# Performance work log

Hardware: AMD Instinct MI355X
Metric: run time of the kernel (lower is better)

## Reference

```python
import jax, jax.numpy as jnp
import numpy as np

B, H, S, D = 1, 16, 2048, 128
NUM_DOCS = 4


def setup_inputs() -> dict:
    key = jax.random.key(0)
    kq, kk, kv = jax.random.split(key, 3)
    q = jax.random.normal(kq, (B, H, S, D), dtype=jnp.float32)
    k = jax.random.normal(kk, (B, H, S, D), dtype=jnp.float32)
    v = jax.random.normal(kv, (B, H, S, D), dtype=jnp.float32)
    # Document boundaries within the packed sequence (as produced by _get_offsets):
    # starts at 0, ends at total token count. 4 equal docs of length 512.
    offsets = jnp.array([0, 512, 1024, 1536, 2048], dtype=jnp.int64)
    return {"q": q, "k": k, "v": v, "offsets": offsets}


def reference(q, k, v, offsets):
    # Block-causal SDPA: token i attends to token j iff j <= i and both are
    # in the same document (documents delimited by `offsets`). This matches
    # nested-tensor SDPA with is_causal=True over the jagged documents.
    _, _, S_, D_ = q.shape
    pos = jnp.arange(S_)
    seg = jnp.searchsorted(offsets, pos, side="right")  # [S] document id per token
    mask = (seg[:, None] == seg[None, :]) & (pos[None, :] <= pos[:, None])  # [S,S]
    scale = 1.0 / jnp.sqrt(jnp.asarray(D_, q.dtype))
    scores = jnp.einsum("bhsd,bhtd->bhst", q, k) * scale  # [B,H,S,S]
    scores = jnp.where(mask[None, None], scores, jnp.finfo(q.dtype).min)
    attn = jax.nn.softmax(scores, axis=-1)
    return jnp.einsum("bhst,bhtd->bhsd", attn, v)
```

## Files before the change

kernel.cpp:

```cpp
#include <hip/hip_runtime.h>
#include <hip/hip_bf16.h>
#include <math.h>

#define NH 16
#define SL 2048
#define DM 128

typedef float f32x4 __attribute__((ext_vector_type(4)));
typedef short s16x8 __attribute__((ext_vector_type(8)));
typedef short s16x4 __attribute__((ext_vector_type(4)));
typedef int   i32x4 __attribute__((ext_vector_type(4)));

static __device__ __forceinline__ unsigned short f2bfu(float f) {
  __hip_bfloat16 h = __float2bfloat16(f);
  return (unsigned short)__builtin_bit_cast(short, h);
}
static __device__ __forceinline__ short f2bf(float f) {
  __hip_bfloat16 h = __float2bfloat16(f);
  return __builtin_bit_cast(short, h);
}
static __device__ __forceinline__ unsigned pack2(float lo, float hi) {
  return (unsigned)f2bfu(lo) | ((unsigned)f2bfu(hi) << 16);
}

__global__ __launch_bounds__(256) void attn_dbuf(
    const float* __restrict__ qg,
    const float* __restrict__ kg,
    const float* __restrict__ vg,
    const int* __restrict__ offs, int n_off,
    float* __restrict__ out)
{
  __shared__ __align__(16) char Kb[2][16384];
  __shared__ __align__(16) char Vb[2][16384];

  const int t    = threadIdx.x;
  const int lane = t & 63;
  const int w    = t >> 6;
  const int col  = lane & 15;
  const int g    = lane >> 4;

  const int blk = blockIdx.x;
  const int z   = blk >> 8;
  const int y   = (blk >> 4) & 15;
  const int h   = blk & 15;
  const int dno = y >> 2, u = y & 3;
  const int p   = z ? u : 7 - u;
  const int q0  = (dno * 8 + p) * 64;

  const float* qh = qg + (size_t)h * SL * DM;
  const float* kh = kg + (size_t)h * SL * DM;
  const float* vh = vg + (size_t)h * SL * DM;

  const float scale2 = 0.08838834764831843f * 1.4426950408889634f;

  const int qrow = q0 + 16 * w + col;

  int ov[8];
  #pragma unroll
  for (int ii = 0; ii < 8; ++ii) ov[ii] = (ii < n_off) ? offs[ii] : 0x7fffffff;
  int qstart = 0, kv_lo = 0;
  #pragma unroll
  for (int ii = 0; ii < 8; ++ii) {
    if (ov[ii] <= qrow) qstart = max(qstart, ov[ii]);
    if (ov[ii] <= q0)   kv_lo  = max(kv_lo, ov[ii]);
  }
  const int n = ((q0 + 64) - kv_lo) >> 6;

  s16x8 qf[4];
  #pragma unroll
  for (int kk = 0; kk < 4; ++kk) {
    const float* qp = qh + (size_t)qrow * DM + 32 * kk + 8 * g;
    f32x4 lo = *(const f32x4*)qp;
    f32x4 hi = *(const f32x4*)(qp + 4);
    s16x8 f;
    f[0] = f2bf(lo[0] * scale2); f[1] = f2bf(lo[1] * scale2);
    f[2] = f2bf(lo[2] * scale2); f[3] = f2bf(lo[3] * scale2);
    f[4] = f2bf(hi[0] * scale2); f[5] = f2bf(hi[1] * scale2);
    f[6] = f2bf(hi[2] * scale2); f[7] = f2bf(hi[3] * scale2);
    qf[kk] = f;
  }

  f32x4 acc[8];
  #pragma unroll
  for (int dt = 0; dt < 8; ++dt) { f32x4 zv = {0.f, 0.f, 0.f, 0.f}; acc[dt] = zv; }
  float m_ = -1e30f, l_ = 0.f;

  const int d0  = (t & 31) * 4;
  const int r0  = t >> 5;
  const int rot = (t >> 1) & 3;
  f32x4 kr[8], vr[8];

#define LOADT(T) do {                                                         \
    const float* _ks = kh + (size_t)(kv_lo + ((T) << 6)) * DM;                \
    const float* _vs = vh + (size_t)(kv_lo + ((T) << 6)) * DM;                \
    _Pragma("unroll")                                                         \
    for (int _i = 0; _i < 8; ++_i)                                            \
      kr[_i] = *(const f32x4*)(_ks + (size_t)(r0 + 8 * _i) * DM + d0);        \
    _Pragma("unroll")                                                         \
    for (int _k = 0; _k < 2; ++_k) {                                          \
      _Pragma("unroll")                                                       \
      for (int _j = 0; _j < 4; ++_j)                                          \
        vr[_k * 4 + _j] =                                                     \
          *(const f32x4*)(_vs + (size_t)(r0 * 4 + 32 * _k + _j) * DM + d0);   \
    }                                                                         \
  } while (0)

#define WRITEKV(B) do {                                                       \
    _Pragma("unroll")                                                         \
    for (int _i = 0; _i < 8; ++_i) {                                          \
      int _r = r0 + 8 * _i;                                                   \
      s16x4 _b;                                                               \
      _b[0] = f2bf(kr[_i][0]); _b[1] = f2bf(kr[_i][1]);                       \
      _b[2] = f2bf(kr[_i][2]); _b[3] = f2bf(kr[_i][3]);                       \
      *(s16x4*)(&Kb[B][0] + ((_r * 256 + d0 * 2) ^ ((_r & 7) << 4))) = _b;    \
    }                                                                         \
    _Pragma("unroll")                                                         \
    for (int _k = 0; _k < 2; ++_k) {                                          \
      int _k0 = r0 * 4 + 32 * _k;                                             \
      _Pragma("unroll")                                                       \
      for (int _di = 0; _di < 4; ++_di) {                                     \
        int _dd = (_di + rot) & 3;                                            \
        int _d  = d0 + _dd;                                                   \
        s16x4 _b;                                                             \
        _b[0] = f2bf(vr[_k * 4 + 0][_dd]); _b[1] = f2bf(vr[_k * 4 + 1][_dd]); \
        _b[2] = f2bf(vr[_k * 4 + 2][_dd]); _b[3] = f2bf(vr[_k * 4 + 3][_dd]); \
        *(s16x4*)(&Vb[B][0] + ((_d * 128 + _k0 * 2) ^ ((_d & 7) << 4))) = _b; \
      }                                                                       \
    }                                                                         \
  } while (0)

  LOADT(0);
  WRITEKV(0);
  int cur = 0;

  const int srcA = col + 32 * (g & 1);
  const int srcB = srcA + 16;
  const bool hi2 = (g >> 1) != 0;

  for (int it = 0; it < n; ++it) {
    const int kv0 = kv_lo + (it << 6);
    __syncthreads();

    const bool pre = (it + 1 < n);
    if (pre) LOADT(it + 1);
    __builtin_amdgcn_sched_barrier(0);

    f32x4 st[4];
    #pragma unroll
    for (int kt = 0; kt < 4; ++kt) { f32x4 zv = {0.f, 0.f, 0.f, 0.f}; st[kt] = zv; }
    __builtin_amdgcn_s_setprio(1);
    #pragma unroll
    for (int kt = 0; kt < 4; ++kt) {
      int row = kt * 16 + col;
      #pragma unroll
      for (int kk = 0; kk < 4; ++kk) {
        s16x8 kf = *(const s16x8*)(&Kb[cur][0] + ((row * 256 + 64 * kk + 16 * g) ^ ((row & 7) << 4)));
        st[kt] = __builtin_amdgcn_mfma_f32_16x16x32_bf16(kf, qf[kk], st[kt], 0, 0, 0);
      }
    }
    __builtin_amdgcn_s_setprio(0);

    const bool needmask = __any((kv0 + 63 > qrow) || (kv0 < qstart));
    if (needmask) {
      #pragma unroll
      for (int kt = 0; kt < 4; ++kt) {
        #pragma unroll
        for (int r = 0; r < 4; ++r) {
          int kpos = kv0 + kt * 16 + 4 * g + r;
          bool ok = (kpos <= qrow) && (kpos >= qstart);
          st[kt][r] = ok ? st[kt][r] : -3.0e38f;
        }
      }
    }
    float cm = -3.0e38f;
    #pragma unroll
    for (int kt = 0; kt < 4; ++kt) {
      #pragma unroll
      for (int r = 0; r < 4; ++r) cm = fmaxf(cm, st[kt][r]);
    }
    cm = fmaxf(cm, __shfl_xor(cm, 16));
    cm = fmaxf(cm, __shfl_xor(cm, 32));
    float al = 1.f;
    float mn = m_;
    if (!__all(cm <= m_)) {
      mn = fmaxf(m_, cm);
      al = __builtin_amdgcn_exp2f(m_ - mn);
      m_ = mn;
      #pragma unroll
      for (int r = 0; r < 4; ++r) {
        float ar = __shfl(al, 4 * g + r);
        #pragma unroll
        for (int dt = 0; dt < 8; ++dt) acc[dt][r] *= ar;
      }
    }
    float psum = 0.f;
    unsigned w01[4], w23[4];
    #pragma unroll
    for (int kt = 0; kt < 4; ++kt) {
      float p0 = __builtin_amdgcn_exp2f(st[kt][0] - mn);
      float p1 = __builtin_amdgcn_exp2f(st[kt][1] - mn);
      float p2 = __builtin_amdgcn_exp2f(st[kt][2] - mn);
      float p3 = __builtin_amdgcn_exp2f(st[kt][3] - mn);
      psum += (p0 + p1) + (p2 + p3);
      w01[kt] = pack2(p0, p1);
      w23[kt] = pack2(p2, p3);
    }
    psum += __shfl_xor(psum, 16);
    psum += __shfl_xor(psum, 32);
    l_ = l_ * al + psum;

    __builtin_amdgcn_s_setprio(1);
    #pragma unroll
    for (int ksel = 0; ksel < 2; ++ksel) {
      unsigned a0 = __shfl(w01[2 * ksel], srcA);
      unsigned a1 = __shfl(w01[2 * ksel + 1], srcA);
      unsigned b0 = __shfl(w23[2 * ksel], srcA);
      unsigned b1 = __shfl(w23[2 * ksel + 1], srcA);
      unsigned c0 = __shfl(w01[2 * ksel], srcB);
      unsigned c1 = __shfl(w01[2 * ksel + 1], srcB);
      unsigned e0 = __shfl(w23[2 * ksel], srcB);
      unsigned e1 = __shfl(w23[2 * ksel + 1], srcB);
      i32x4 uu;
      uu[0] = (int)(hi2 ? a1 : a0);
      uu[1] = (int)(hi2 ? b1 : b0);
      uu[2] = (int)(hi2 ? c1 : c0);
      uu[3] = (int)(hi2 ? e1 : e0);
      s16x8 pa = __builtin_bit_cast(s16x8, uu);
      #pragma unroll
      for (int dt = 0; dt < 8; ++dt) {
        int d = dt * 16 + col;
        s16x8 vf = *(const s16x8*)(&Vb[cur][0] + ((d * 128 + 64 * ksel + 16 * g) ^ ((d & 7) << 4)));
        acc[dt] = __builtin_amdgcn_mfma_f32_16x16x32_bf16(pa, vf, acc[dt], 0, 0, 0);
      }
    }
    __builtin_amdgcn_s_setprio(0);

    if (pre) WRITEKV(cur ^ 1);
    cur ^= 1;
  }
#undef LOADT
#undef WRITEKV

  #pragma unroll
  for (int r = 0; r < 4; ++r) {
    float lr  = __shfl(l_, 4 * g + r);
    float inv = 1.f / lr;
    int row   = q0 + 16 * w + 4 * g + r;
    float* op = out + ((size_t)h * SL + row) * DM + col;
    #pragma unroll
    for (int dt = 0; dt < 8; ++dt) op[dt * 16] = acc[dt][r] * inv;
  }
}

extern "C" void kernel_launch(void* const* d_in, const int* in_sizes, int n_in,
                              void* d_out, int out_size, void* d_ws, size_t ws_size,
                              hipStream_t stream) {
  const float* q = (const float*)d_in[0];
  const float* k = (const float*)d_in[1];
  const float* v = (const float*)d_in[2];
  const int* offs = (const int*)d_in[3];
  const int n_off = in_sizes[3];
  float* out = (float*)d_out;

  const int blocks = NH * (SL / 64);
  attn_dbuf<<<blocks, 256, 0, stream>>>(q, k, v, offs, n_off, out);
}
```

Measured before the change: 28.43 us.

## Process 128 query rows per block with 512 threads sharing KV tiles

Each block now handles a 128-row query tile with 8 waves instead of 64 rows with 4 waves, so every staged 64-row K/V tile in shared memory serves twice as many queries and global K/V traffic and conversion work per query are halved. The cooperative load is split across 512 threads, with each thread loading fewer rows. The block count halves and the launch order changes from a balanced causal pairing to descending query-block order. Diagonal tiles now cover more masked work per block, and the smaller grid may reduce occupancy and load balance.

```diff
diff --git a/kernel.cpp b/kernel.cpp
--- a/kernel.cpp
+++ b/kernel.cpp
@@ -23,7 +23,7 @@
   return (unsigned)f2bfu(lo) | ((unsigned)f2bfu(hi) << 16);
 }
 
-__global__ __launch_bounds__(256) void attn_dbuf(
+__global__ __launch_bounds__(512) void attn_bq128(
     const float* __restrict__ qg,
     const float* __restrict__ kg,
     const float* __restrict__ vg,
@@ -39,13 +39,10 @@
   const int col  = lane & 15;
   const int g    = lane >> 4;
 
-  const int blk = blockIdx.x;
-  const int z   = blk >> 8;
-  const int y   = (blk >> 4) & 15;
-  const int h   = blk & 15;
-  const int dno = y >> 2, u = y & 3;
-  const int p   = z ? u : 7 - u;
-  const int q0  = (dno * 8 + p) * 64;
+  const int b  = blockIdx.x;
+  const int h  = b & 15;
+  const int qb = 15 - (b >> 4);
+  const int q0 = qb * 128;
 
   const float* qh = qg + (size_t)h * SL * DM;
   const float* kh = kg + (size_t)h * SL * DM;
@@ -64,7 +61,7 @@
     if (ov[ii] <= qrow) qstart = max(qstart, ov[ii]);
     if (ov[ii] <= q0)   kv_lo  = max(kv_lo, ov[ii]);
   }
-  const int n = ((q0 + 64) - kv_lo) >> 6;
+  const int n = ((q0 + 128) - kv_lo) >> 6;
 
   s16x8 qf[4];
   #pragma unroll
@@ -87,45 +84,38 @@
 
   const int d0  = (t & 31) * 4;
   const int r0  = t >> 5;
+  const int k0  = r0 * 4;
   const int rot = (t >> 1) & 3;
-  f32x4 kr[8], vr[8];
+  f32x4 kr[4], vr[4];
 
 #define LOADT(T) do {                                                         \
     const float* _ks = kh + (size_t)(kv_lo + ((T) << 6)) * DM;                \
     const float* _vs = vh + (size_t)(kv_lo + ((T) << 6)) * DM;                \
     _Pragma("unroll")                                                         \
-    for (int _i = 0; _i < 8; ++_i)                                            \
-      kr[_i] = *(const f32x4*)(_ks + (size_t)(r0 + 8 * _i) * DM + d0);        \
-    _Pragma("unroll")                                                         \
-    for (int _k = 0; _k < 2; ++_k) {                                          \
-      _Pragma("unroll")                                                       \
-      for (int _j = 0; _j < 4; ++_j)                                          \
-        vr[_k * 4 + _j] =                                                     \
-          *(const f32x4*)(_vs + (size_t)(r0 * 4 + 32 * _k + _j) * DM + d0);   \
-    }                                                                         \
+    for (int _i = 0; _i < 4; ++_i)                                            \
+      kr[_i] = *(const f32x4*)(_ks + (size_t)(r0 + 16 * _i) * DM + d0);       \
+    _Pragma("unroll")                                                         \
+    for (int _j = 0; _j < 4; ++_j)                                            \
+      vr[_j] = *(const f32x4*)(_vs + (size_t)(k0 + _j) * DM + d0);            \
   } while (0)
 
 #define WRITEKV(B) do {                                                       \
     _Pragma("unroll")                                                         \
-    for (int _i = 0; _i < 8; ++_i) {                                          \
-      int _r = r0 + 8 * _i;                                                   \
+    for (int _i = 0; _i < 4; ++_i) {                                          \
+      int _r = r0 + 16 * _i;                                                  \
       s16x4 _b;                                                               \
       _b[0] = f2bf(kr[_i][0]); _b[1] = f2bf(kr[_i][1]);                       \
       _b[2] = f2bf(kr[_i][2]); _b[3] = f2bf(kr[_i][3]);                       \
       *(s16x4*)(&Kb[B][0] + ((_r * 256 + d0 * 2) ^ ((_r & 7) << 4))) = _b;    \
     }                                                                         \
     _Pragma("unroll")                                                         \
-    for (int _k = 0; _k < 2; ++_k) {                                          \
-      int _k0 = r0 * 4 + 32 * _k;                                             \
-      _Pragma("unroll")                                                       \
-      for (int _di = 0; _di < 4; ++_di) {                                     \
-        int _dd = (_di + rot) & 3;                                            \
-        int _d  = d0 + _dd;                                                   \
-        s16x4 _b;                                                             \
-        _b[0] = f2bf(vr[_k * 4 + 0][_dd]); _b[1] = f2bf(vr[_k * 4 + 1][_dd]); \
-        _b[2] = f2bf(vr[_k * 4 + 2][_dd]); _b[3] = f2bf(vr[_k * 4 + 3][_dd]); \
-        *(s16x4*)(&Vb[B][0] + ((_d * 128 + _k0 * 2) ^ ((_d & 7) << 4))) = _b; \
-      }                                                                       \
+    for (int _di = 0; _di < 4; ++_di) {                                       \
+      int _dd = (_di + rot) & 3;                                              \
+      int _d  = d0 + _dd;                                                     \
+      s16x4 _b;                                                               \
+      _b[0] = f2bf(vr[0][_dd]); _b[1] = f2bf(vr[1][_dd]);                     \
+      _b[2] = f2bf(vr[2][_dd]); _b[3] = f2bf(vr[3][_dd]);                     \
+      *(s16x4*)(&Vb[B][0] + ((_d * 128 + k0 * 2) ^ ((_d & 7) << 4))) = _b;    \
     }                                                                         \
   } while (0)
 
@@ -262,6 +252,6 @@
   const int n_off = in_sizes[3];
   float* out = (float*)d_out;
 
-  const int blocks = NH * (SL / 64);
-  attn_dbuf<<<blocks, 256, 0, stream>>>(q, k, v, offs, n_off, out);
-}
+  const int blocks = NH * (SL / 128);
+  attn_bq128<<<blocks, 512, 0, stream>>>(q, k, v, offs, n_off, out);
+}
```

Result: slower. 30.01 us (+5.6%).
